# Kernel optimization log

Hardware: AMD Instinct MI355X
Metric: run time of the kernel (lower is better)

## Reference

```python
import jax, jax.numpy as jnp
import numpy as np

B, T, IN, H, OUT = 1024, 1024, 1, 20, 2
G = 4 * H  # gate dim (i, f, g, o order as in PyTorch)


def setup_inputs() -> dict:
    key = jax.random.key(0)
    ks = jax.random.split(key, 16)
    s = 1.0 / np.sqrt(H)  # PyTorch default uniform(-1/sqrt(H), 1/sqrt(H)) scale
    def u(k, shape):
        return jax.random.uniform(k, shape, jnp.float32, -s, s)
    inp = {"x": jax.random.normal(ks[0], (B, T, IN), jnp.float32)}
    ins = [IN, H, H]
    i = 1
    for l in range(3):
        inp[f"w_ih{l}"] = u(ks[i], (G, ins[l])); i += 1
        inp[f"w_hh{l}"] = u(ks[i], (G, H)); i += 1
        inp[f"b_ih{l}"] = u(ks[i], (G,)); i += 1
        inp[f"b_hh{l}"] = u(ks[i], (G,)); i += 1
    inp["fc_w"] = u(ks[13], (OUT, H))
    inp["fc_b"] = u(ks[14], (OUT,))
    return inp


def _lstm_layer(x, w_ih, w_hh, b_ih, b_hh):
    # x: [B, T, in] -> hidden sequence [B, T, H]
    b, t, _ = x.shape
    h = w_hh.shape[1]
    # Precompute input contribution for all timesteps (vectorized over T).
    xg = jnp.einsum('bti,gi->btg', x, w_ih) + b_ih + b_hh  # [B, T, 4H]

    def step(carry, xg_t):
        hp, cp = carry
        gates = xg_t + hp @ w_hh.T  # [B, 4H]
        i, f, g, o = jnp.split(gates, 4, axis=-1)
        c = jax.nn.sigmoid(f) * cp + jax.nn.sigmoid(i) * jnp.tanh(g)
        hn = jax.nn.sigmoid(o) * jnp.tanh(c)
        return (hn, c), hn

    h0 = jnp.zeros((b, h), x.dtype)
    (_, _), hs = jax.lax.scan(step, (h0, h0), jnp.swapaxes(xg, 0, 1))
    return jnp.swapaxes(hs, 0, 1)  # [B, T, H]


def reference(x, w_ih0, w_hh0, b_ih0, b_hh0, w_ih1, w_hh1, b_ih1, b_hh1,
              w_ih2, w_hh2, b_ih2, b_hh2, fc_w, fc_b):
    y = _lstm_layer(x, w_ih0, w_hh0, b_ih0, b_hh0)
    y = _lstm_layer(y, w_ih1, w_hh1, b_ih1, b_hh1)
    y = _lstm_layer(y, w_ih2, w_hh2, b_ih2, b_hh2)
    return y[:, -1, :] @ fc_w.T + fc_b  # [B, OUT]
```

## Files before the change

kernel.cpp:

```cpp
#include <hip/hip_runtime.h>

typedef _Float16 half2v __attribute__((ext_vector_type(2)));
typedef _Float16 f16x8  __attribute__((ext_vector_type(8)));
typedef float    f32x4  __attribute__((ext_vector_type(4)));

#define T_LEN 1024
#define NBATCH 1024
#define HID 20
#define G_B 2
#define STEPS 16
#define RSLOT 64
#define PPITCH 84

#if defined(__has_builtin)
#if __has_builtin(__builtin_amdgcn_fdot2)
#define HAVE_FDOT2 1
#endif
#endif

#define NLOG2E  -1.4426950408889634f
#define N2LOG2E -2.8853900817779268f

__device__ __forceinline__ float fdot2_(half2v a, half2v b, float c) {
#ifdef HAVE_FDOT2
    return __builtin_amdgcn_fdot2(a, b, c, false);
#else
    return c + (float)a[0] * (float)b[0] + (float)a[1] * (float)b[1];
#endif
}

__device__ __forceinline__ half2v pack2(float a, float b) {
    half2v r; r[0] = (_Float16)a; r[1] = (_Float16)b; return r;
}

__device__ __forceinline__ void load_h20(const _Float16* row, half2v hp[10]) {
    uint4 q0 = *(const uint4*)(row);
    uint4 q1 = *(const uint4*)(row + 8);
    uint2 q2 = *(const uint2*)(row + 16);
    hp[0] = __builtin_bit_cast(half2v, q0.x);
    hp[1] = __builtin_bit_cast(half2v, q0.y);
    hp[2] = __builtin_bit_cast(half2v, q0.z);
    hp[3] = __builtin_bit_cast(half2v, q0.w);
    hp[4] = __builtin_bit_cast(half2v, q1.x);
    hp[5] = __builtin_bit_cast(half2v, q1.y);
    hp[6] = __builtin_bit_cast(half2v, q1.z);
    hp[7] = __builtin_bit_cast(half2v, q1.w);
    hp[8] = __builtin_bit_cast(half2v, q2.x);
    hp[9] = __builtin_bit_cast(half2v, q2.y);
}

__device__ __forceinline__ float dot20s(const half2v W[10], const half2v h[10],
                                        float seed) {
    float a0 = seed, a1 = 0.f;
#pragma unroll
    for (int k = 0; k < 5; ++k) {
        a0 = fdot2_(W[k],     h[k],     a0);
        a1 = fdot2_(W[k + 5], h[k + 5], a1);
    }
    return a0 + a1;
}

__global__ void __launch_bounds__(192, 2) lstm3_r18(
    const float* __restrict__ x,
    const float* __restrict__ wih0, const float* __restrict__ whh0,
    const float* __restrict__ bih0, const float* __restrict__ bhh0,
    const float* __restrict__ wih1, const float* __restrict__ whh1,
    const float* __restrict__ bih1, const float* __restrict__ bhh1,
    const float* __restrict__ wih2, const float* __restrict__ whh2,
    const float* __restrict__ bih2, const float* __restrict__ bhh2,
    const float* __restrict__ fcw, const float* __restrict__ fcb,
    float* __restrict__ out)
{
    __shared__ __align__(16) float xlds[G_B * T_LEN];
    __shared__ __align__(16) _Float16 rings[3][2 * STEPS][RSLOT];
    __shared__ __align__(16) float plds[2][2 * STEPS][PPITCH];

    const int tid = threadIdx.x;
    const int wv = tid / 64;
    const int lane = tid & 63;
    const long b_base = (long)blockIdx.x * G_B;

    {
        const float* xg = x + b_base * T_LEN;
        for (int i = tid; i < G_B * T_LEN; i += 192) {
            const int t = i & (T_LEN - 1);
            const int g = i >> 10;
            xlds[2 * t + g] = xg[i];
        }
        for (int i = tid; i < 3 * 2 * STEPS * RSLOT; i += 192)
            ((_Float16*)rings)[i] = (_Float16)0.0f;
    }

    const bool act = lane < G_B * HID;
    const int g = act ? (lane / HID) : 0;
    const int j = act ? (lane % HID) : 0;

    const float* whh = (wv == 0) ? whh0 : (wv == 1) ? whh1 : whh2;
    const float* wih = (wv == 0) ? wih0 : (wv == 1) ? wih1 : wih2;
    const float* bih = (wv == 0) ? bih0 : (wv == 1) ? bih1 : bih2;
    const float* bhh = (wv == 0) ? bhh0 : (wv == 1) ? bhh1 : bhh2;

    half2v Whh[4][10];
    float bias[4];
    float wx[4] = {0.f, 0.f, 0.f, 0.f};
#pragma unroll
    for (int gt = 0; gt < 4; ++gt) {
        const float sc = (gt == 2) ? N2LOG2E : NLOG2E;
        const int r = gt * HID + j;
#pragma unroll
        for (int k4 = 0; k4 < 5; ++k4) {
            float4 v = *(const float4*)(whh + r * HID + 4 * k4);
            Whh[gt][2 * k4]     = pack2(sc * v.x, sc * v.y);
            Whh[gt][2 * k4 + 1] = pack2(sc * v.z, sc * v.w);
        }
        bias[gt] = sc * (bih[r] + bhh[r]);
        if (wv == 0) wx[gt] = sc * wih[r];
    }

    f16x8 WihB[5];
    int col4[5];
    if (wv > 0) {
        const int kc = (lane >> 4) * 8;
        const int col = lane & 15;
#pragma unroll
        for (int t = 0; t < 5; ++t) {
            const int n = t * 16 + col;
            const int gt = n / HID;
            const float sc = (gt == 2) ? N2LOG2E : NLOG2E;
            f16x8 v;
#pragma unroll
            for (int e = 0; e < 8; ++e) {
                const int k = kc + e;
                const float w = (k < HID) ? wih[n * HID + k] : 0.f;
                v[e] = (_Float16)(sc * w);
            }
            WihB[t] = v;
            col4[t] = (n % HID) * 4 + gt;
        }
    }

    _Float16* const own_base = &rings[wv][0][0];
    const _Float16* const bel_base = (wv > 0) ? &rings[wv - 1][0][0]
                                              : &rings[0][0][0];
    float* const myp = &plds[(wv > 0) ? (wv - 1) : 0][0][0];
    const float* const prb = myp + g * PPITCH + 4 * j;

    float c = 0.0f;
    float oA[4] = {bias[0], bias[1], bias[2], bias[3]};

    __syncthreads();

    const int SS = T_LEN / STEPS;

    for (int s = 0; s < SS + 2; ++s) {
        const int m = s - wv;
        if (m >= 0 && m < SS) {
            const int t0 = STEPS * m;
            const int hb = (m & 1) * (STEPS * RSLOT);

            float xr[STEPS];
            f32x4 pf[STEPS];

            if (wv > 0) {
                const int ar = lane & 15;
                const int kc = (lane >> 4) * 8;
                const int crow = (lane >> 4) * 4;
                const f32x4 z = {0.f, 0.f, 0.f, 0.f};
#pragma unroll
                for (int h = 0; h < 2; ++h) {
                    const _Float16* ab = bel_base + hb
                        + ((ar >> 1) + 8 * h) * RSLOT + (ar & 1) * 32 + kc;
                    const f16x8 af = *(const f16x8*)ab;
#pragma unroll
                    for (int t = 0; t < 5; ++t) {
                        f32x4 acc = __builtin_amdgcn_mfma_f32_16x16x32_f16(
                            af, WihB[t], z, 0, 0, 0);
                        float* wrow = myp + (crow + 16 * h) * PPITCH + col4[t];
#pragma unroll
                        for (int q = 0; q < 4; ++q)
                            wrow[q * PPITCH] = acc[q];
                    }
                }
#pragma unroll
                for (int i = 0; i < STEPS; ++i)
                    pf[i] = *(const f32x4*)(prb + 2 * i * PPITCH);
            } else {
                const float* xp = xlds + 2 * t0 + g;
#pragma unroll
                for (int i = 0; i < STEPS; ++i)
                    xr[i] = xp[2 * i];
            }

            const int qo = hb + g * 32;
#pragma unroll
            for (int i = 0; i < STEPS; ++i) {
                float p[4];
                if (wv == 0) {
#pragma unroll
                    for (int gt = 0; gt < 4; ++gt)
                        p[gt] = oA[gt] + wx[gt] * xr[i];
                } else {
#pragma unroll
                    for (int gt = 0; gt < 4; ++gt)
                        p[gt] = oA[gt] + pf[i][gt];
                }
                const float ei = __builtin_exp2f(p[0]);
                const float ef = __builtin_exp2f(p[1]);
                const float eg = __builtin_exp2f(p[2]);
                const float eo = __builtin_exp2f(p[3]);
                const float sf = __builtin_amdgcn_rcpf(1.0f + ef);
                const float u  = (1.0f - eg) *
                    __builtin_amdgcn_rcpf((1.0f + ei) * (1.0f + eg));
                c = sf * c + u;
                const float ec = __builtin_exp2f(N2LOG2E * c);
                const float hn = (1.0f - ec) *
                    __builtin_amdgcn_rcpf((1.0f + eo) * (1.0f + ec));
                _Float16* const wp = own_base + qo + i * RSLOT;
                if (act) wp[j] = (_Float16)hn;
                half2v ho[10];
                load_h20(wp, ho);
#pragma unroll
                for (int gt = 0; gt < 4; ++gt)
                    oA[gt] = dot20s(Whh[gt], ho, bias[gt]);
            }
        }
        __syncthreads();
    }

    if (wv == 2 && lane < 2 * G_B) {
        const int gg = lane >> 1, o = lane & 1;
        float acc = fcb[o];
        const _Float16* h2 = &rings[2][2 * STEPS - 1][gg * 32];
#pragma unroll
        for (int k = 0; k < HID; ++k) {
            acc += fcw[o * HID + k] * (float)h2[k];
        }
        out[(b_base + gg) * 2 + o] = acc;
    }
}

extern "C" void kernel_launch(void* const* d_in, const int* in_sizes, int n_in,
                              void* d_out, int out_size, void* d_ws, size_t ws_size,
                              hipStream_t stream) {
    const float* x    = (const float*)d_in[0];
    const float* wih0 = (const float*)d_in[1];
    const float* whh0 = (const float*)d_in[2];
    const float* bih0 = (const float*)d_in[3];
    const float* bhh0 = (const float*)d_in[4];
    const float* wih1 = (const float*)d_in[5];
    const float* whh1 = (const float*)d_in[6];
    const float* bih1 = (const float*)d_in[7];
    const float* bhh1 = (const float*)d_in[8];
    const float* wih2 = (const float*)d_in[9];
    const float* whh2 = (const float*)d_in[10];
    const float* bih2 = (const float*)d_in[11];
    const float* bhh2 = (const float*)d_in[12];
    const float* fcw  = (const float*)d_in[13];
    const float* fcb  = (const float*)d_in[14];

    lstm3_r18<<<dim3(NBATCH / G_B), dim3(192), 0, stream>>>(
        x, wih0, whh0, bih0, bhh0,
        wih1, whh1, bih1, bhh1,
        wih2, whh2, bih2, bhh2,
        fcw, fcb, (float*)d_out);
}
```

Measured before the change: 557.8 us.

## Process two batch rows per lane and four per block for ILP

Each lane now advances two independent LSTM recurrences (batch rows) interleaved, with blocks covering four batch rows and half as many blocks launched. Ring and projection buffers are widened accordingly and the MFMA input-projection covers four rows. The intent is to hide the latency of the serial exp/rcp/dot chain with independent work, at the cost of more registers, one block per CU, and more LDS traffic per step.

After: 639.4 us. +14.6%, slower.

```diff
diff --git a/kernel.cpp b/kernel.cpp
--- a/kernel.cpp
+++ b/kernel.cpp
@@ -7,9 +7,9 @@
 #define T_LEN 1024
 #define NBATCH 1024
 #define HID 20
-#define G_B 2
+#define G_B 4
 #define STEPS 16
-#define RSLOT 64
+#define RSLOT 128
 #define PPITCH 84
 
 #if defined(__has_builtin)
@@ -60,7 +60,22 @@
     return a0 + a1;
 }
 
-__global__ void __launch_bounds__(192, 2) lstm3_r18(
+__device__ __forceinline__ float lstm_cell(float p0, float p1, float p2,
+                                           float p3, float& c) {
+    const float ei = __builtin_exp2f(p0);
+    const float ef = __builtin_exp2f(p1);
+    const float eg = __builtin_exp2f(p2);
+    const float eo = __builtin_exp2f(p3);
+    const float sf = __builtin_amdgcn_rcpf(1.0f + ef);
+    const float u  = (1.0f - eg) *
+        __builtin_amdgcn_rcpf((1.0f + ei) * (1.0f + eg));
+    c = sf * c + u;
+    const float ec = __builtin_exp2f(N2LOG2E * c);
+    return (1.0f - ec) *
+        __builtin_amdgcn_rcpf((1.0f + eo) * (1.0f + ec));
+}
+
+__global__ void __launch_bounds__(192, 1) lstm3_r23(
     const float* __restrict__ x,
     const float* __restrict__ wih0, const float* __restrict__ whh0,
     const float* __restrict__ bih0, const float* __restrict__ bhh0,
@@ -73,7 +88,7 @@
 {
     __shared__ __align__(16) float xlds[G_B * T_LEN];
     __shared__ __align__(16) _Float16 rings[3][2 * STEPS][RSLOT];
-    __shared__ __align__(16) float plds[2][2 * STEPS][PPITCH];
+    __shared__ __align__(16) float plds[2][4 * STEPS][PPITCH];
 
     const int tid = threadIdx.x;
     const int wv = tid / 64;
@@ -84,16 +99,19 @@
         const float* xg = x + b_base * T_LEN;
         for (int i = tid; i < G_B * T_LEN; i += 192) {
             const int t = i & (T_LEN - 1);
-            const int g = i >> 10;
-            xlds[2 * t + g] = xg[i];
+            const int b = i >> 10;
+            xlds[4 * t + b] = xg[i];
         }
         for (int i = tid; i < 3 * 2 * STEPS * RSLOT; i += 192)
             ((_Float16*)rings)[i] = (_Float16)0.0f;
     }
 
-    const bool act = lane < G_B * HID;
-    const int g = act ? (lane / HID) : 0;
-    const int j = act ? (lane % HID) : 0;
+    const int pr = lane >> 5;
+    const int lj = lane & 31;
+    const bool act = lj < HID;
+    const int j = act ? lj : 0;
+    const int b0 = 2 * pr;
+    const int b1 = 2 * pr + 1;
 
     const float* whh = (wv == 0) ? whh0 : (wv == 1) ? whh1 : whh2;
     const float* wih = (wv == 0) ? wih0 : (wv == 1) ? wih1 : wih2;
@@ -143,10 +161,12 @@
     const _Float16* const bel_base = (wv > 0) ? &rings[wv - 1][0][0]
                                               : &rings[0][0][0];
     float* const myp = &plds[(wv > 0) ? (wv - 1) : 0][0][0];
-    const float* const prb = myp + g * PPITCH + 4 * j;
-
-    float c = 0.0f;
-    float oA[4] = {bias[0], bias[1], bias[2], bias[3]};
+    const float* const prb0 = myp + b0 * PPITCH + 4 * j;
+    const float* const prb1 = myp + b1 * PPITCH + 4 * j;
+
+    float c0 = 0.0f, c1 = 0.0f;
+    float oA0[4] = {bias[0], bias[1], bias[2], bias[3]};
+    float oA1[4] = {bias[0], bias[1], bias[2], bias[3]};
 
     __syncthreads();
 
@@ -158,8 +178,7 @@
             const int t0 = STEPS * m;
             const int hb = (m & 1) * (STEPS * RSLOT);
 
-            float xr[STEPS];
-            f32x4 pf[STEPS];
+            float xr0[STEPS], xr1[STEPS];
 
             if (wv > 0) {
                 const int ar = lane & 15;
@@ -167,9 +186,9 @@
                 const int crow = (lane >> 4) * 4;
                 const f32x4 z = {0.f, 0.f, 0.f, 0.f};
 #pragma unroll
-                for (int h = 0; h < 2; ++h) {
+                for (int h = 0; h < 4; ++h) {
                     const _Float16* ab = bel_base + hb
-                        + ((ar >> 1) + 8 * h) * RSLOT + (ar & 1) * 32 + kc;
+                        + (4 * h + (ar >> 2)) * RSLOT + (ar & 3) * 32 + kc;
                     const f16x8 af = *(const f16x8*)ab;
 #pragma unroll
                     for (int t = 0; t < 5; ++t) {
@@ -181,47 +200,52 @@
                             wrow[q * PPITCH] = acc[q];
                     }
                 }
-#pragma unroll
-                for (int i = 0; i < STEPS; ++i)
-                    pf[i] = *(const f32x4*)(prb + 2 * i * PPITCH);
             } else {
-                const float* xp = xlds + 2 * t0 + g;
-#pragma unroll
-                for (int i = 0; i < STEPS; ++i)
-                    xr[i] = xp[2 * i];
+                const float* xp = xlds + 4 * t0;
+#pragma unroll
+                for (int i = 0; i < STEPS; ++i) {
+                    xr0[i] = xp[4 * i + b0];
+                    xr1[i] = xp[4 * i + b1];
+                }
             }
 
-            const int qo = hb + g * 32;
+            const int qo0 = hb + b0 * 32;
+            const int qo1 = hb + b1 * 32;
 #pragma unroll
             for (int i = 0; i < STEPS; ++i) {
-                float p[4];
+                float p0[4], p1[4];
                 if (wv == 0) {
 #pragma unroll
-                    for (int gt = 0; gt < 4; ++gt)
-                        p[gt] = oA[gt] + wx[gt] * xr[i];
+                    for (int gt = 0; gt < 4; ++gt) {
+                        p0[gt] = oA0[gt] + wx[gt] * xr0[i];
+                        p1[gt] = oA1[gt] + wx[gt] * xr1[i];
+                    }
                 } else {
-#pragma unroll
-                    for (int gt = 0; gt < 4; ++gt)
-                        p[gt] = oA[gt] + pf[i][gt];
+                    const f32x4 pf0 = *(const f32x4*)(prb0 + 4 * i * PPITCH);
+                    const f32x4 pf1 = *(const f32x4*)(prb1 + 4 * i * PPITCH);
+#pragma unroll
+                    for (int gt = 0; gt < 4; ++gt) {
+                        p0[gt] = oA0[gt] + pf0[gt];
+                        p1[gt] = oA1[gt] + pf1[gt];
+                    }
                 }
-                const float ei = __builtin_exp2f(p[0]);
-                const float ef = __builtin_exp2f(p[1]);
-                const float eg = __builtin_exp2f(p[2]);
-                const float eo = __builtin_exp2f(p[3]);
-                const float sf = __builtin_amdgcn_rcpf(1.0f + ef);
-                const float u  = (1.0f - eg) *
-                    __builtin_amdgcn_rcpf((1.0f + ei) * (1.0f + eg));
-                c = sf * c + u;
-                const float ec = __builtin_exp2f(N2LOG2E * c);
-                const float hn = (1.0f - ec) *
-                    __builtin_amdgcn_rcpf((1.0f + eo) * (1.0f + ec));
-                _Float16* const wp = own_base + qo + i * RSLOT;
-                if (act) wp[j] = (_Float16)hn;
-                half2v ho[10];
-                load_h20(wp, ho);
+                const float hn0 = lstm_cell(p0[0], p0[1], p0[2], p0[3], c0);
+                const float hn1 = lstm_cell(p1[0], p1[1], p1[2], p1[3], c1);
+
+                const _Float16 hf0 = (_Float16)hn0;
+                const _Float16 hf1 = (_Float16)hn1;
+                _Float16* const sp = own_base + i * RSLOT;
+                if (act) sp[qo0 + j] = hf0;
+                if (act) sp[qo1 + j] = hf1;
+                half2v ho0[10], ho1[10];
+                load_h20(sp + qo0, ho0);
+                load_h20(sp + qo1, ho1);
 #pragma unroll
                 for (int gt = 0; gt < 4; ++gt)
-                    oA[gt] = dot20s(Whh[gt], ho, bias[gt]);
+                    oA0[gt] = dot20s(Whh[gt], ho0, bias[gt]);
+#pragma unroll
+                for (int gt = 0; gt < 4; ++gt)
+                    oA1[gt] = dot20s(Whh[gt], ho1, bias[gt]);
             }
         }
         __syncthreads();
@@ -258,7 +282,7 @@
     const float* fcw  = (const float*)d_in[13];
     const float* fcb  = (const float*)d_in[14];
 
-    lstm3_r18<<<dim3(NBATCH / G_B), dim3(192), 0, stream>>>(
+    lstm3_r23<<<dim3(NBATCH / G_B), dim3(192), 0, stream>>>(
         x, wih0, whh0, bih0, bhh0,
         wih1, whh1, bih1, bhh1,
         wih2, whh2, bih2, bhh2,
```

## Process one batch element per block to double grid parallelism

Applied to the files above, without the earlier changes.

Each block now handles a single batch row instead of two, so the grid doubles to 1024 blocks and the launch bound allows three blocks per CU. Each wave uses 20 active lanes instead of 40, the LDS ring and projection buffers shrink, and the MFMA input projection drops from two row-halves to one. The aim is to shorten the serial recurrence per block and raise occupancy, at the cost of half-empty waves and MFMA tiles that are now only partly used.

Result: slower. 949.7 us (+70.3%).

```diff
diff --git a/kernel.cpp b/kernel.cpp
--- a/kernel.cpp
+++ b/kernel.cpp
@@ -7,9 +7,9 @@
 #define T_LEN 1024
 #define NBATCH 1024
 #define HID 20
-#define G_B 2
+#define G_B 1
 #define STEPS 16
-#define RSLOT 64
+#define RSLOT 32
 #define PPITCH 84
 
 #if defined(__has_builtin)
@@ -60,7 +60,7 @@
     return a0 + a1;
 }
 
-__global__ void __launch_bounds__(192, 2) lstm3_r18(
+__global__ void __launch_bounds__(192, 3) lstm3_r24(
     const float* __restrict__ x,
     const float* __restrict__ wih0, const float* __restrict__ whh0,
     const float* __restrict__ bih0, const float* __restrict__ bhh0,
@@ -71,29 +71,25 @@
     const float* __restrict__ fcw, const float* __restrict__ fcb,
     float* __restrict__ out)
 {
-    __shared__ __align__(16) float xlds[G_B * T_LEN];
+    __shared__ __align__(16) float xlds[T_LEN];
     __shared__ __align__(16) _Float16 rings[3][2 * STEPS][RSLOT];
-    __shared__ __align__(16) float plds[2][2 * STEPS][PPITCH];
+    __shared__ __align__(16) float plds[2][STEPS][PPITCH];
 
     const int tid = threadIdx.x;
     const int wv = tid / 64;
     const int lane = tid & 63;
-    const long b_base = (long)blockIdx.x * G_B;
+    const long b = blockIdx.x;
 
     {
-        const float* xg = x + b_base * T_LEN;
-        for (int i = tid; i < G_B * T_LEN; i += 192) {
-            const int t = i & (T_LEN - 1);
-            const int g = i >> 10;
-            xlds[2 * t + g] = xg[i];
-        }
+        const float* xg = x + b * T_LEN;
+        for (int i = tid; i < T_LEN; i += 192)
+            xlds[i] = xg[i];
         for (int i = tid; i < 3 * 2 * STEPS * RSLOT; i += 192)
             ((_Float16*)rings)[i] = (_Float16)0.0f;
     }
 
-    const bool act = lane < G_B * HID;
-    const int g = act ? (lane / HID) : 0;
-    const int j = act ? (lane % HID) : 0;
+    const bool act = lane < HID;
+    const int j = act ? lane : 0;
 
     const float* whh = (wv == 0) ? whh0 : (wv == 1) ? whh1 : whh2;
     const float* wih = (wv == 0) ? wih0 : (wv == 1) ? wih1 : wih2;
@@ -143,7 +139,7 @@
     const _Float16* const bel_base = (wv > 0) ? &rings[wv - 1][0][0]
                                               : &rings[0][0][0];
     float* const myp = &plds[(wv > 0) ? (wv - 1) : 0][0][0];
-    const float* const prb = myp + g * PPITCH + 4 * j;
+    const float* const prb = myp + 4 * j;
 
     float c = 0.0f;
     float oA[4] = {bias[0], bias[1], bias[2], bias[3]};
@@ -166,32 +162,27 @@
                 const int kc = (lane >> 4) * 8;
                 const int crow = (lane >> 4) * 4;
                 const f32x4 z = {0.f, 0.f, 0.f, 0.f};
-#pragma unroll
-                for (int h = 0; h < 2; ++h) {
-                    const _Float16* ab = bel_base + hb
-                        + ((ar >> 1) + 8 * h) * RSLOT + (ar & 1) * 32 + kc;
-                    const f16x8 af = *(const f16x8*)ab;
-#pragma unroll
-                    for (int t = 0; t < 5; ++t) {
-                        f32x4 acc = __builtin_amdgcn_mfma_f32_16x16x32_f16(
-                            af, WihB[t], z, 0, 0, 0);
-                        float* wrow = myp + (crow + 16 * h) * PPITCH + col4[t];
-#pragma unroll
-                        for (int q = 0; q < 4; ++q)
-                            wrow[q * PPITCH] = acc[q];
-                    }
+                const _Float16* ab = bel_base + hb + ar * RSLOT + kc;
+                const f16x8 af = *(const f16x8*)ab;
+#pragma unroll
+                for (int t = 0; t < 5; ++t) {
+                    f32x4 acc = __builtin_amdgcn_mfma_f32_16x16x32_f16(
+                        af, WihB[t], z, 0, 0, 0);
+                    float* wrow = myp + crow * PPITCH + col4[t];
+#pragma unroll
+                    for (int q = 0; q < 4; ++q)
+                        wrow[q * PPITCH] = acc[q];
                 }
 #pragma unroll
                 for (int i = 0; i < STEPS; ++i)
-                    pf[i] = *(const f32x4*)(prb + 2 * i * PPITCH);
+                    pf[i] = *(const f32x4*)(prb + i * PPITCH);
             } else {
-                const float* xp = xlds + 2 * t0 + g;
+                const float* xp = xlds + t0;
 #pragma unroll
                 for (int i = 0; i < STEPS; ++i)
-                    xr[i] = xp[2 * i];
+                    xr[i] = xp[i];
             }
 
-            const int qo = hb + g * 32;
 #pragma unroll
             for (int i = 0; i < STEPS; ++i) {
                 float p[4];
@@ -215,7 +206,8 @@
                 const float ec = __builtin_exp2f(N2LOG2E * c);
                 const float hn = (1.0f - ec) *
                     __builtin_amdgcn_rcpf((1.0f + eo) * (1.0f + ec));
-                _Float16* const wp = own_base + qo + i * RSLOT;
+
+                _Float16* const wp = own_base + hb + i * RSLOT;
                 if (act) wp[j] = (_Float16)hn;
                 half2v ho[10];
                 load_h20(wp, ho);
@@ -227,15 +219,15 @@
         __syncthreads();
     }
 
-    if (wv == 2 && lane < 2 * G_B) {
-        const int gg = lane >> 1, o = lane & 1;
+    if (wv == 2 && lane < 2) {
+        const int o = lane;
         float acc = fcb[o];
-        const _Float16* h2 = &rings[2][2 * STEPS - 1][gg * 32];
+        const _Float16* h2 = &rings[2][2 * STEPS - 1][0];
 #pragma unroll
         for (int k = 0; k < HID; ++k) {
             acc += fcw[o * HID + k] * (float)h2[k];
         }
-        out[(b_base + gg) * 2 + o] = acc;
+        out[b * 2 + o] = acc;
     }
 }
 
@@ -258,7 +250,7 @@
     const float* fcw  = (const float*)d_in[13];
     const float* fcb  = (const float*)d_in[14];
 
-    lstm3_r18<<<dim3(NBATCH / G_B), dim3(192), 0, stream>>>(
+    lstm3_r24<<<dim3(NBATCH), dim3(192), 0, stream>>>(
         x, wih0, whh0, bih0, bhh0,
         wih1, whh1, bih1, bhh1,
         wih2, whh2, bih2, bhh2,
```
